# Optimization experiments

Measured on AMD Instinct MI355X. Metric: run time of the kernel, lower is better.

Reference implementation:

```python
import jax, jax.numpy as jnp
import numpy as np

EPS = 1e-5

def setup_inputs() -> dict:
    key = jax.random.key(0)
    ks = jax.random.split(key, 8)
    B, C, H, W = 16, 512, 41, 41
    N = H * W
    Ck = C // 2
    return {
        "x": jax.random.normal(ks[0], (B, C, H, W), jnp.float32),
        "fg_sim": jax.random.uniform(ks[1], (B, N, N), jnp.float32),
        "bg_sim": jax.random.uniform(ks[2], (B, N, N), jnp.float32),
        "Wq": jax.random.normal(ks[3], (Ck, C), jnp.float32) * 0.02,
        "bq": jax.random.normal(ks[4], (Ck,), jnp.float32) * 0.02,
        "Wk": jax.random.normal(ks[5], (Ck, C), jnp.float32) * 0.02,
        "bk": jax.random.normal(ks[6], (Ck,), jnp.float32) * 0.02,
        "gamma": jax.random.normal(ks[7], (1,), jnp.float32) * 0.1,
    }

def reference(x, fg_sim, bg_sim, Wq, bq, Wk, bk, gamma):
    B, C, H, W = x.shape
    N = H * W
    Ck = Wk.shape[0]
    xf = x.reshape(B, C, N)                       # [B, C, N]
    # 1x1 convs = channel matmuls
    query = jnp.einsum('kc,bcn->bnk', Wq, xf) + bq  # [B, N, Ck]
    key_ = jnp.einsum('kc,bcn->bkn', Wk, xf) + bk[None, :, None]  # [B, Ck, N]
    sim = jnp.einsum('bnk,bkm->bnm', query, key_) * (Ck ** -0.5)  # [B, N, N]
    sim = sim * fg_sim
    # masked_normalize: min-subtract, mask, sum-normalize
    min_v = jnp.min(sim, axis=-1, keepdims=True)
    x1 = (sim - min_v) * fg_sim
    sim = x1 / (jnp.sum(x1, axis=-1, keepdims=True) + EPS)
    sim = sim + bg_sim
    value = xf.transpose(0, 2, 1)                 # [B, N, C]
    context = jnp.einsum('bnm,bmc->bnc', sim, value)  # [B, N, C]
    context = context.transpose(0, 2, 1).reshape(B, C, H, W)
    fuse = gamma[0] * context + x
    return fuse
```

## Files before the change

### kernel.cpp

```cpp
#include <hip/hip_runtime.h>
#include <math.h>

#define B_   16
#define C_   512
#define N_   1681
#define Np   1792
#define CK_  256
#define EPSV 1e-5f
#define SCALE 0.0625f

typedef __bf16 bf16x8 __attribute__((ext_vector_type(8)));
typedef float  f32x4  __attribute__((ext_vector_type(4)));

__device__ __forceinline__
void stage_tile(const char* gbase, int ld_bytes, char* lds, int w, int lane)
{
    #pragma unroll
    for (int i = 0; i < 4; ++i) {
        int chunk = (i * 4 + w) * 64 + lane;
        int row   = chunk >> 3;
        int col   = chunk & 7;
        int scol  = col ^ (row & 7);
        const char* g = gbase + (size_t)row * ld_bytes + scol * 16;
        char* l = lds + (size_t)(i * 4 + w) * 1024;
        __builtin_amdgcn_global_load_lds(
            (const __attribute__((address_space(1))) void*)g,
            (__attribute__((address_space(3))) void*)l, 16, 0, 0);
    }
}

__device__ __forceinline__
void mma_tile(const __bf16* As, const __bf16* Bs, f32x4 acc[4][4], int wr, int wc, int lane)
{
    const int l15 = lane & 15, quad = lane >> 4;
    #pragma unroll
    for (int kk = 0; kk < 2; ++kk) {
        bf16x8 af[4], bfr[4];
        #pragma unroll
        for (int i = 0; i < 4; ++i) {
            int row = wr * 64 + i * 16 + l15;
            int c   = (kk * 4 + quad) ^ (row & 7);
            af[i] = *(const bf16x8*)(As + row * 64 + c * 8);
        }
        #pragma unroll
        for (int j = 0; j < 4; ++j) {
            int row = wc * 64 + j * 16 + l15;
            int c   = (kk * 4 + quad) ^ (row & 7);
            bfr[j] = *(const bf16x8*)(Bs + row * 64 + c * 8);
        }
        #pragma unroll
        for (int i = 0; i < 4; ++i)
            #pragma unroll
            for (int j = 0; j < 4; ++j)
                acc[i][j] = __builtin_amdgcn_mfma_f32_16x16x32_bf16(
                    af[i], bfr[j], acc[i][j], 0, 0, 0);
    }
}

__global__ __launch_bounds__(256)
void cvt_w_kernel(const float* __restrict__ Wq, const float* __restrict__ Wk,
                  const float* __restrict__ bq, const float* __restrict__ bk,
                  __bf16* __restrict__ Wh, float* __restrict__ b2)
{
    int idx = blockIdx.x * 1024 + threadIdx.x * 4;
    #pragma unroll
    for (int p = 0; p < 4; ++p) {
        int e = idx + p;
        int row = e >> 9, col = e & 511;
        float v = (row < 256) ? Wq[row * 512 + col] : Wk[(row - 256) * 512 + col];
        Wh[e] = (__bf16)v;
    }
    if (blockIdx.x == 0) {
        int t = threadIdx.x;
        b2[t]       = bq[t];
        b2[256 + t] = bk[t];
    }
}

__global__ __launch_bounds__(256)
void cvt_x_kernel(const float* __restrict__ x,
                  __bf16* __restrict__ xh, __bf16* __restrict__ xt)
{
    __shared__ float tile[32][33];
    const int t = threadIdx.x;
    const int n0 = blockIdx.x * 32, c0 = blockIdx.y * 32, b = blockIdx.z;
    const float* xb = x + (size_t)b * C_ * N_;
    #pragma unroll
    for (int p = 0; p < 4; ++p) {
        int lin = p * 256 + t;
        int i = lin >> 5, j = lin & 31;
        int n = n0 + j;
        float v = (n < N_) ? xb[(size_t)(c0 + i) * N_ + n] : 0.0f;
        tile[i][j] = v;
        xh[(size_t)b * C_ * Np + (size_t)(c0 + i) * Np + n] = (__bf16)v;
    }
    __syncthreads();
    #pragma unroll
    for (int p = 0; p < 4; ++p) {
        int lin = p * 256 + t;
        int i = lin >> 5, j = lin & 31;
        xt[(size_t)b * Np * C_ + (size_t)(n0 + i) * C_ + (c0 + j)] = (__bf16)tile[j][i];
    }
}

__global__ __launch_bounds__(256)
void proj_kernel(const __bf16* __restrict__ xt, const __bf16* __restrict__ Wh,
                 const float* __restrict__ b2, __bf16* __restrict__ QKt)
{
    __shared__ __bf16 As[128 * 64];
    __shared__ __bf16 Bs[128 * 64];
    const int t = threadIdx.x, w = t >> 6, lane = t & 63;
    const int n0 = blockIdx.x * 128, k20 = blockIdx.y * 128, b = blockIdx.z;
    const char* Abase = (const char*)xt + ((size_t)b * Np + n0) * (C_ * 2);
    const char* Bbase = (const char*)Wh + (size_t)k20 * (C_ * 2);

    f32x4 acc[4][4] = {};
    for (int k0 = 0; k0 < C_; k0 += 64) {
        stage_tile(Abase + k0 * 2, C_ * 2, (char*)As, w, lane);
        stage_tile(Bbase + k0 * 2, C_ * 2, (char*)Bs, w, lane);
        __syncthreads();
        mma_tile(As, Bs, acc, w >> 1, w & 1, lane);
        __syncthreads();
    }
    const int l15 = lane & 15, quad = lane >> 4;
    __bf16* ob = QKt + (size_t)b * Np * 512;
    #pragma unroll
    for (int j = 0; j < 4; ++j) {
        int k2 = k20 + (w & 1) * 64 + j * 16 + l15;
        float bias = b2[k2];
        #pragma unroll
        for (int i = 0; i < 4; ++i)
            #pragma unroll
            for (int r = 0; r < 4; ++r) {
                int n = n0 + (w >> 1) * 64 + i * 16 + quad * 4 + r;
                ob[(size_t)n * 512 + k2] = (__bf16)(acc[i][j][r] + bias);
            }
    }
}

__global__ __launch_bounds__(256)
void sim_kernel(const __bf16* __restrict__ QKt, __bf16* __restrict__ S)
{
    __shared__ __bf16 As[128 * 64];
    __shared__ __bf16 Bs[128 * 64];
    const int t = threadIdx.x, w = t >> 6, lane = t & 63;
    const int m0 = blockIdx.x * 128, n0 = blockIdx.y * 128, b = blockIdx.z;
    const char* base = (const char*)QKt + (size_t)b * Np * 1024;
    const char* Abase = base + (size_t)n0 * 1024;
    const char* Bbase = base + (size_t)m0 * 1024 + 512;

    f32x4 acc[4][4] = {};
    for (int k0 = 0; k0 < CK_; k0 += 64) {
        stage_tile(Abase + k0 * 2, 1024, (char*)As, w, lane);
        stage_tile(Bbase + k0 * 2, 1024, (char*)Bs, w, lane);
        __syncthreads();
        mma_tile(As, Bs, acc, w >> 1, w & 1, lane);
        __syncthreads();
    }
    const int l15 = lane & 15, quad = lane >> 4;
    __bf16* Sb = S + (size_t)b * Np * Np;
    #pragma unroll
    for (int i = 0; i < 4; ++i)
        #pragma unroll
        for (int r = 0; r < 4; ++r) {
            int n = n0 + (w >> 1) * 64 + i * 16 + quad * 4 + r;
            #pragma unroll
            for (int j = 0; j < 4; ++j) {
                int m = m0 + (w & 1) * 64 + j * 16 + l15;
                Sb[(size_t)n * Np + m] = (__bf16)(acc[i][j][r] * SCALE);
            }
        }
}

__global__ __launch_bounds__(256)
void norm_kernel(const float* __restrict__ fg, const float* __restrict__ bg,
                 __bf16* __restrict__ S)
{
    __shared__ float sx[N_];
    __shared__ float sf[N_];
    __shared__ float red[8];
    const int t = threadIdx.x, n = blockIdx.x, b = blockIdx.y;
    __bf16* Srow = S + (size_t)b * Np * Np + (size_t)n * Np;
    const float* fgrow = fg + ((size_t)b * N_ + n) * N_;
    const float* bgrow = bg + ((size_t)b * N_ + n) * N_;

    float lmin = INFINITY;
    for (int m = t; m < N_; m += 256) {
        float fv = fgrow[m];
        float sv = (float)Srow[m] * fv;
        sx[m] = sv; sf[m] = fv;
        lmin = fminf(lmin, sv);
    }
    #pragma unroll
    for (int off = 32; off > 0; off >>= 1)
        lmin = fminf(lmin, __shfl_down(lmin, off, 64));
    const int wid = t >> 6;
    if ((t & 63) == 0) red[wid] = lmin;
    __syncthreads();
    const float minv = fminf(fminf(red[0], red[1]), fminf(red[2], red[3]));

    float lsum = 0.0f;
    for (int m = t; m < N_; m += 256) {
        float x1 = (sx[m] - minv) * sf[m];
        sx[m] = x1;
        lsum += x1;
    }
    #pragma unroll
    for (int off = 32; off > 0; off >>= 1)
        lsum += __shfl_down(lsum, off, 64);
    if ((t & 63) == 0) red[4 + wid] = lsum;
    __syncthreads();
    const float inv = 1.0f / (red[4] + red[5] + red[6] + red[7] + EPSV);

    for (int m = t; m < N_; m += 256)
        Srow[m] = (__bf16)(sx[m] * inv + bgrow[m]);
    for (int m = N_ + t; m < Np; m += 256)
        Srow[m] = (__bf16)0.0f;
}

__global__ __launch_bounds__(256)
void ctx_kernel(const __bf16* __restrict__ xh, const __bf16* __restrict__ Ap,
                const float* __restrict__ x, const float* __restrict__ gamma,
                float* __restrict__ out)
{
    __shared__ __bf16 As[128 * 64];
    __shared__ __bf16 Bs[128 * 64];
    const int t = threadIdx.x, w = t >> 6, lane = t & 63;
    const int c0 = blockIdx.x * 128, n0 = blockIdx.y * 128, b = blockIdx.z;
    const char* Abase = (const char*)xh + ((size_t)b * C_ + c0) * (Np * 2);
    const char* Bbase = (const char*)Ap + ((size_t)b * Np + n0) * (Np * 2);

    f32x4 acc[4][4] = {};
    for (int k0 = 0; k0 < Np; k0 += 64) {
        stage_tile(Abase + k0 * 2, Np * 2, (char*)As, w, lane);
        stage_tile(Bbase + k0 * 2, Np * 2, (char*)Bs, w, lane);
        __syncthreads();
        mma_tile(As, Bs, acc, w >> 1, w & 1, lane);
        __syncthreads();
    }
    const int l15 = lane & 15, quad = lane >> 4;
    const float g = gamma[0];
    const float* xb = x + (size_t)b * C_ * N_;
    float* ob = out + (size_t)b * C_ * N_;
    #pragma unroll
    for (int i = 0; i < 4; ++i)
        #pragma unroll
        for (int r = 0; r < 4; ++r) {
            int c = c0 + (w >> 1) * 64 + i * 16 + quad * 4 + r;
            #pragma unroll
            for (int j = 0; j < 4; ++j) {
                int n = n0 + (w & 1) * 64 + j * 16 + l15;
                if (n < N_) {
                    size_t idx = (size_t)c * N_ + n;
                    ob[idx] = g * acc[i][j][r] + xb[idx];
                }
            }
        }
}

extern "C" void kernel_launch(void* const* d_in, const int* in_sizes, int n_in,
                              void* d_out, int out_size, void* d_ws, size_t ws_size,
                              hipStream_t stream)
{
    const float* x     = (const float*)d_in[0];
    const float* fg    = (const float*)d_in[1];
    const float* bg    = (const float*)d_in[2];
    const float* Wq    = (const float*)d_in[3];
    const float* bq    = (const float*)d_in[4];
    const float* Wk    = (const float*)d_in[5];
    const float* bk    = (const float*)d_in[6];
    const float* gamma = (const float*)d_in[7];
    float* out = (float*)d_out;

    char* p = (char*)d_ws;
    __bf16* xh  = (__bf16*)p; p += (size_t)B_ * C_ * Np * 2;
    __bf16* xt  = (__bf16*)p; p += (size_t)B_ * Np * C_ * 2;
    __bf16* QKt = (__bf16*)p; p += (size_t)B_ * Np * 512 * 2;
    __bf16* S   = (__bf16*)p; p += (size_t)B_ * Np * Np * 2;
    __bf16* Wh  = (__bf16*)p; p += (size_t)512 * 512 * 2;
    float*  b2  = (float*)p;

    cvt_w_kernel<<<dim3(256), dim3(256), 0, stream>>>(Wq, Wk, bq, bk, Wh, b2);
    cvt_x_kernel<<<dim3(Np / 32, C_ / 32, B_), dim3(256), 0, stream>>>(x, xh, xt);
    proj_kernel<<<dim3(Np / 128, 4, B_), dim3(256), 0, stream>>>(xt, Wh, b2, QKt);
    sim_kernel<<<dim3(Np / 128, Np / 128, B_), dim3(256), 0, stream>>>(QKt, S);
    norm_kernel<<<dim3(N_, B_), dim3(256), 0, stream>>>(fg, bg, S);
    ctx_kernel<<<dim3(C_ / 128, Np / 128, B_), dim3(256), 0, stream>>>(xh, S, x, gamma, out);
}
```

Baseline: 697.8 us.

## Rewrite masked normalize as one-wave-per-row register kernel with single-pass reduction

The normalization kernel now gives each row to one 64-lane wavefront instead of a full 256-thread block. Each lane keeps its values in registers rather than LDS and loads four elements per access. The min and sum reductions are merged into one butterfly pass using the identity sum((s-min)*f) = sum(s*f) - min*sum(f). This removes LDS traffic, block barriers and a second reduction, but the algebraic rewrite can lose precision through cancellation. The float4 loads of fg and bg rows are only 4-byte aligned because the row length is odd.

Result: faster. 662.1 us (-5.1%).

```diff
diff --git a/kernel.cpp b/kernel.cpp
--- a/kernel.cpp
+++ b/kernel.cpp
@@ -10,6 +10,7 @@
 #define SCALE 0.0625f
 
 typedef __bf16 bf16x8 __attribute__((ext_vector_type(8)));
+typedef __bf16 bf16x4 __attribute__((ext_vector_type(4)));
 typedef float  f32x4  __attribute__((ext_vector_type(4)));
 
 __device__ __forceinline__
@@ -172,50 +173,79 @@
         }
 }
 
-__global__ __launch_bounds__(256)
+__global__ __launch_bounds__(256, 4)
 void norm_kernel(const float* __restrict__ fg, const float* __restrict__ bg,
                  __bf16* __restrict__ S)
 {
-    __shared__ float sx[N_];
-    __shared__ float sf[N_];
-    __shared__ float red[8];
-    const int t = threadIdx.x, n = blockIdx.x, b = blockIdx.y;
+    const int t = threadIdx.x;
+    const int wid = t >> 6, lane = t & 63;
+    const int n = blockIdx.x * 4 + wid;
+    const int b = blockIdx.y;
+    if (n >= N_) return;
+
     __bf16* Srow = S + (size_t)b * Np * Np + (size_t)n * Np;
     const float* fgrow = fg + ((size_t)b * N_ + n) * N_;
     const float* bgrow = bg + ((size_t)b * N_ + n) * N_;
 
-    float lmin = INFINITY;
-    for (int m = t; m < N_; m += 256) {
-        float fv = fgrow[m];
-        float sv = (float)Srow[m] * fv;
-        sx[m] = sv; sf[m] = fv;
-        lmin = fminf(lmin, sv);
-    }
-    #pragma unroll
-    for (int off = 32; off > 0; off >>= 1)
-        lmin = fminf(lmin, __shfl_down(lmin, off, 64));
-    const int wid = t >> 6;
-    if ((t & 63) == 0) red[wid] = lmin;
-    __syncthreads();
-    const float minv = fminf(fminf(red[0], red[1]), fminf(red[2], red[3]));
-
-    float lsum = 0.0f;
-    for (int m = t; m < N_; m += 256) {
-        float x1 = (sx[m] - minv) * sf[m];
-        sx[m] = x1;
-        lsum += x1;
-    }
-    #pragma unroll
-    for (int off = 32; off > 0; off >>= 1)
-        lsum += __shfl_down(lsum, off, 64);
-    if ((t & 63) == 0) red[4 + wid] = lsum;
-    __syncthreads();
-    const float inv = 1.0f / (red[4] + red[5] + red[6] + red[7] + EPSV);
-
-    for (int m = t; m < N_; m += 256)
-        Srow[m] = (__bf16)(sx[m] * inv + bgrow[m]);
-    for (int m = N_ + t; m < Np; m += 256)
-        Srow[m] = (__bf16)0.0f;
+    float sv[7][4];
+    float fv[7][4];
+    float lmin = INFINITY, aSum = 0.0f, fSum = 0.0f;
+
+    #pragma unroll
+    for (int i = 0; i < 7; ++i) {
+        const int m0 = i * 256 + lane * 4;
+        bf16x4 sr = *(const bf16x4*)(Srow + m0);
+        f32x4 f;
+        if (m0 + 4 <= N_) {
+            f = *(const f32x4*)(fgrow + m0);
+        } else {
+            f[0] = (m0 + 0 < N_) ? fgrow[m0 + 0] : 0.0f;
+            f[1] = (m0 + 1 < N_) ? fgrow[m0 + 1] : 0.0f;
+            f[2] = (m0 + 2 < N_) ? fgrow[m0 + 2] : 0.0f;
+            f[3] = (m0 + 3 < N_) ? fgrow[m0 + 3] : 0.0f;
+        }
+        #pragma unroll
+        for (int k = 0; k < 4; ++k) {
+            const bool valid = (m0 + k) < N_;
+            const float fk = f[k];
+            const float svk = (float)sr[k] * fk;
+            sv[i][k] = svk;
+            fv[i][k] = fk;
+            aSum += svk * fk;
+            fSum += fk;
+            lmin = fminf(lmin, valid ? svk : INFINITY);
+        }
+    }
+
+    #pragma unroll
+    for (int off = 1; off < 64; off <<= 1) {
+        lmin = fminf(lmin, __shfl_xor(lmin, off, 64));
+        aSum += __shfl_xor(aSum, off, 64);
+        fSum += __shfl_xor(fSum, off, 64);
+    }
+    const float inv = 1.0f / ((aSum - lmin * fSum) + EPSV);
+
+    #pragma unroll
+    for (int i = 0; i < 7; ++i) {
+        const int m0 = i * 256 + lane * 4;
+        f32x4 g;
+        if (m0 + 4 <= N_) {
+            g = *(const f32x4*)(bgrow + m0);
+        } else {
+            g[0] = (m0 + 0 < N_) ? bgrow[m0 + 0] : 0.0f;
+            g[1] = (m0 + 1 < N_) ? bgrow[m0 + 1] : 0.0f;
+            g[2] = (m0 + 2 < N_) ? bgrow[m0 + 2] : 0.0f;
+            g[3] = (m0 + 3 < N_) ? bgrow[m0 + 3] : 0.0f;
+        }
+        bf16x4 o;
+        #pragma unroll
+        for (int k = 0; k < 4; ++k) {
+            const bool valid = (m0 + k) < N_;
+            const float x1 = (sv[i][k] - lmin) * fv[i][k];
+            o[k] = (__bf16)(valid ? (x1 * inv + g[k]) : 0.0f);
+        }
+        *(bf16x4*)(Srow + m0) = o;
+    }
 }
 
 __global__ __launch_bounds__(256)
@@ -284,6 +314,6 @@
     cvt_x_kernel<<<dim3(Np / 32, C_ / 32, B_), dim3(256), 0, stream>>>(x, xh, xt);
     proj_kernel<<<dim3(Np / 128, 4, B_), dim3(256), 0, stream>>>(xt, Wh, b2, QKt);
     sim_kernel<<<dim3(Np / 128, Np / 128, B_), dim3(256), 0, stream>>>(QKt, S);
-    norm_kernel<<<dim3(N_, B_), dim3(256), 0, stream>>>(fg, bg, S);
+    norm_kernel<<<dim3((N_ + 3) / 4, B_), dim3(256), 0, stream>>>(fg, bg, S);
     ctx_kernel<<<dim3(C_ / 128, Np / 128, B_), dim3(256), 0, stream>>>(xh, S, x, gamma, out);
 }
```
